# Kernel tuning notes

Measured on AMD Instinct MI355X. Metric: run time of the kernel, lower is better.

## Reference

```python
import jax, jax.numpy as jnp
import numpy as np

N = 262144      # total line-graph nodes (16 graphs x 16384)
E = 2097152     # total line-graph edges (avg degree 8)
F_IN = 8        # edge_attr feature dim
FEATURES_DIM = 64


def gcn_conv(x, src, dst, W, b, n):
    """PyG GCNConv: x' = D^{-1/2} (A+I) D^{-1/2} (x W) + b, deg from in-edges incl. self-loops."""
    x = x @ W
    loop = jnp.arange(n, dtype=src.dtype)
    si = jnp.concatenate([src, loop])
    di = jnp.concatenate([dst, loop])
    deg = jax.ops.segment_sum(jnp.ones(si.shape[0], dtype=x.dtype), di, num_segments=n)
    dinv = jnp.where(deg > 0, deg ** -0.5, 0.0)
    norm = dinv[si] * dinv[di]                      # [E+N]
    msg = x[si] * norm[:, None]                     # gather + scale
    return jax.ops.segment_sum(msg, di, num_segments=n) + b


def setup_inputs() -> dict:
    key = jax.random.key(0)
    ks = jax.random.split(key, 10)

    def lin(k, fan_in, fan_out):
        return jax.random.normal(k, (fan_in, fan_out), jnp.float32) * (1.0 / np.sqrt(fan_in))

    return {
        "x": jax.random.normal(ks[0], (N, F_IN), jnp.float32),
        "W1": lin(ks[1], F_IN, 16), "b1": jnp.zeros((16,), jnp.float32),
        "W2": lin(ks[2], 16, 32),   "b2": jnp.zeros((32,), jnp.float32),
        "W3": lin(ks[3], 32, 64),   "b3": jnp.zeros((64,), jnp.float32),
        "Wfc": lin(ks[4], 64, FEATURES_DIM), "bfc": jnp.zeros((FEATURES_DIM,), jnp.float32),
        "edge_index": jax.random.randint(ks[5], (2, E), 0, N, dtype=jnp.int32),
        "batch_size": 16,
    }


def reference(x, W1, b1, W2, b2, W3, b3, Wfc, bfc, edge_index, batch_size):
    src, dst = edge_index[0], edge_index[1]
    n = x.shape[0]
    h = jax.nn.relu(gcn_conv(x, src, dst, W1, b1, n))
    h = jax.nn.relu(gcn_conv(h, src, dst, W2, b2, n))
    h = jax.nn.relu(gcn_conv(h, src, dst, W3, b3, n))
    out = h @ Wfc + bfc
    return out.reshape(batch_size, -1, FEATURES_DIM)
```

## Files before the change

### kernel.cpp

```cpp
#include <hip/hip_runtime.h>
#include <hip/hip_bf16.h>


#define NB   256
#define NPB  1024
#define TILE 4096
#define SRCMASK 0x3FFFFu

typedef _Float16 half8 __attribute__((ext_vector_type(8)));
typedef float float4v __attribute__((ext_vector_type(4)));
typedef unsigned int u32x4 __attribute__((ext_vector_type(4)));

__device__ __forceinline__ unsigned pkh(float a, float b) {
    unsigned short ua = __builtin_bit_cast(unsigned short, (_Float16)a);
    unsigned short ub = __builtin_bit_cast(unsigned short, (_Float16)b);
    return (unsigned)ua | ((unsigned)ub << 16);
}
__device__ __forceinline__ float h_lo(unsigned u) {
    return (float)__builtin_bit_cast(_Float16, (unsigned short)(u & 0xFFFFu));
}
__device__ __forceinline__ float h_hi(unsigned u) {
    return (float)__builtin_bit_cast(_Float16, (unsigned short)(u >> 16));
}
__device__ __forceinline__ int ld_nt(const int* p) { return __builtin_nontemporal_load(p); }

#define UNPK8_ADD(A, u) \
    A##0 += h_lo(u.x); A##1 += h_hi(u.x); A##2 += h_lo(u.y); A##3 += h_hi(u.y); \
    A##4 += h_lo(u.z); A##5 += h_hi(u.z); A##6 += h_lo(u.w); A##7 += h_hi(u.w);

__global__ void hist_kernel(const int* __restrict__ dst, int* __restrict__ ghist,
                            int E, int shift) {
    __shared__ int h[NB];
    int tid = threadIdx.x;
    h[tid] = 0;
    __syncthreads();
    int base = blockIdx.x * TILE;
    int cnt = min(TILE, E - base);
    for (int i = tid; i < cnt; i += 256)
        atomicAdd(&h[dst[base + i] >> shift], 1);
    __syncthreads();
    int v = h[tid];
    if (v) atomicAdd(&ghist[tid], v);
}

__global__ void bscan_kernel(const int* __restrict__ ghist, int* __restrict__ bbase,
                             int* __restrict__ gcursor,
                             const float* __restrict__ W3, const float* __restrict__ Wf,
                             _Float16* __restrict__ w3f, _Float16* __restrict__ wff) {
    __shared__ int sh[NB];
    int tid = threadIdx.x;
    int v = ghist[tid];
    sh[tid] = v;
    __syncthreads();
    for (int o = 1; o < NB; o <<= 1) {
        int t = (tid >= o) ? sh[tid - o] : 0;
        __syncthreads();
        sh[tid] += t;
        __syncthreads();
    }
    int incl = sh[tid];
    bbase[tid] = incl - v;
    gcursor[tid] = incl - v;
    if (tid == NB - 1) bbase[NB] = incl;
    for (int i = tid; i < 32 * 64; i += NB) {
        int k = i >> 6, j = i & 63;
        w3f[(j >> 4) * 512 + (j & 15) * 32 + (k >> 3) * 8 + (k & 7)] = (_Float16)W3[i];
    }
    for (int i = tid; i < 64 * 64; i += NB) {
        int k = i >> 6, j = i & 63;
        wff[((k >> 5) * 4 + (j >> 4)) * 512 + (j & 15) * 32 + ((k >> 3) & 3) * 8 + (k & 7)]
            = (_Float16)Wf[i];
    }
}

__global__ void __launch_bounds__(256)
partition_kernel(const int* __restrict__ src, const int* __restrict__ dst,
                 int* __restrict__ gcursor, unsigned int* __restrict__ bedge,
                 int E, int shift, int mask) {
    __shared__ int h[NB], st[NB], gp[NB];
    __shared__ unsigned short rk[TILE];
    __shared__ int sd[TILE];
    __shared__ int ss[TILE];
    int tid = threadIdx.x;
    h[tid] = 0;
    __syncthreads();
    int base = blockIdx.x * TILE;
    int cnt = min(TILE, E - base);
    for (int i = tid; i < cnt; i += 256)
        rk[i] = (unsigned short)atomicAdd(&h[dst[base + i] >> shift], 1);
    __syncthreads();
    int hv = h[tid];
    st[tid] = hv;
    __syncthreads();
    for (int o = 1; o < NB; o <<= 1) {
        int t = (tid >= o) ? st[tid - o] : 0;
        __syncthreads();
        st[tid] += t;
        __syncthreads();
    }
    st[tid] -= hv;
    gp[tid] = hv ? atomicAdd(&gcursor[tid], hv) : 0;
    __syncthreads();
    for (int i = tid; i < cnt; i += 256) {
        int d = dst[base + i];
        int b = d >> shift;
        int pos = st[b] + rk[i];
        sd[pos] = d;
        ss[pos] = src[base + i];
    }
    __syncthreads();
    for (int i = tid; i < cnt; i += 256) {
        int d = sd[i];
        int b = d >> shift;
        int g = gp[b] + (i - st[b]);
        bedge[g] = (unsigned int)ss[i] | ((unsigned int)(d & mask) << 18);
    }
}

__global__ void __launch_bounds__(256)
build_kernel(const int* __restrict__ bbase, const unsigned int* __restrict__ bedge,
             const float* __restrict__ x,
             int* __restrict__ off, float* __restrict__ dinv, int* __restrict__ adj,
             _Float16* __restrict__ y0h) {
    __shared__ int deg1[NPB];
    __shared__ int cur[NPB];
    __shared__ int bs[256];
    int tid = threadIdx.x;
    int b = blockIdx.x;
    int s = bbase[b], e = bbase[b + 1];
    int base = tid * 4;
#pragma unroll
    for (int i = 0; i < 4; i++) deg1[base + i] = 0;
    __syncthreads();
    for (int i = s + tid; i < e; i += 256)
        atomicAdd(&deg1[bedge[i] >> 18], 1);
    __syncthreads();
    int d0 = deg1[base], d1 = deg1[base + 1], d2 = deg1[base + 2], d3 = deg1[base + 3];
    int th = d0 + d1 + d2 + d3;
    bs[tid] = th;
    __syncthreads();
    for (int o = 1; o < 256; o <<= 1) {
        int t = (tid >= o) ? bs[tid - o] : 0;
        __syncthreads();
        bs[tid] += t;
        __syncthreads();
    }
    int run = s + bs[tid] - th;
    int vb = b * NPB + base;
    off[vb]     = run; cur[base]     = run; dinv[vb]     = rsqrtf((float)(d0 + 1)); run += d0;
    off[vb + 1] = run; cur[base + 1] = run; dinv[vb + 1] = rsqrtf((float)(d1 + 1)); run += d1;
    off[vb + 2] = run; cur[base + 2] = run; dinv[vb + 2] = rsqrtf((float)(d2 + 1)); run += d2;
    off[vb + 3] = run; cur[base + 3] = run; dinv[vb + 3] = rsqrtf((float)(d3 + 1)); run += d3;
    if (b == NB - 1 && tid == 255) off[NB * NPB] = e;
    __syncthreads();
    for (int i = s + tid; i < e; i += 256) {
        unsigned int pk = bedge[i];
        int p = atomicAdd(&cur[pk >> 18], 1);
        adj[p] = (int)(pk & SRCMASK);
    }
    for (int i = tid; i < NPB; i += 256) {
        float dv = rsqrtf((float)(deg1[i] + 1));
        const float4* xr = (const float4*)x + (size_t)(b * NPB + i) * 2;
        float4 t0 = xr[0], t1 = xr[1];
        uint4 pk;
        pk.x = pkh(t0.x * dv, t0.y * dv); pk.y = pkh(t0.z * dv, t0.w * dv);
        pk.z = pkh(t1.x * dv, t1.y * dv); pk.w = pkh(t1.z * dv, t1.w * dv);
        ((uint4*)y0h)[(size_t)b * NPB + i] = pk;
    }
}

__global__ void __launch_bounds__(256)
aggt1_kernel(const _Float16* __restrict__ y0h, const int* __restrict__ off,
             const int* __restrict__ adj, const float* __restrict__ dinv,
             const float* __restrict__ W1, const float* __restrict__ b1,
             _Float16* __restrict__ y1h) {
    __shared__ float Ws[8 * 16];
    __shared__ float bsh[16];
    const int tid = threadIdx.x;
    if (tid < 128) Ws[tid] = W1[tid];
    if (tid < 16) bsh[tid] = b1[tid];
    const int vg = blockIdx.x * 256 + tid;
    const u32x4* y4 = (const u32x4*)y0h;
    int beg = off[vg], end = off[vg + 1];
    u32x4 us = y4[vg];
    float a0 = h_lo(us.x), a1 = h_hi(us.x), a2 = h_lo(us.y), a3 = h_hi(us.y),
          a4 = h_lo(us.z), a5 = h_hi(us.z), a6 = h_lo(us.w), a7 = h_hi(us.w);
    float c0 = 0, c1 = 0, c2 = 0, c3 = 0, c4 = 0, c5 = 0, c6 = 0, c7 = 0;
    u32x4 zz; zz.x = 0; zz.y = 0; zz.z = 0; zz.w = 0;
    for (int eb = beg; eb < end; eb += 8) {
        int i0 = ld_nt(adj + eb);
        int i1 = ld_nt(adj + min(eb + 1, end - 1));
        int i2 = ld_nt(adj + min(eb + 2, end - 1));
        int i3 = ld_nt(adj + min(eb + 3, end - 1));
        int i4 = ld_nt(adj + min(eb + 4, end - 1));
        int i5 = ld_nt(adj + min(eb + 5, end - 1));
        int i6 = ld_nt(adj + min(eb + 6, end - 1));
        int i7 = ld_nt(adj + min(eb + 7, end - 1));
        u32x4 u0 = y4[i0], u1 = y4[i1], u2 = y4[i2], u3 = y4[i3];
        u32x4 u4 = y4[i4], u5 = y4[i5], u6 = y4[i6], u7 = y4[i7];
        u1 = (eb + 1 < end) ? u1 : zz;
        u2 = (eb + 2 < end) ? u2 : zz;
        u3 = (eb + 3 < end) ? u3 : zz;
        u4 = (eb + 4 < end) ? u4 : zz;
        u5 = (eb + 5 < end) ? u5 : zz;
        u6 = (eb + 6 < end) ? u6 : zz;
        u7 = (eb + 7 < end) ? u7 : zz;
        UNPK8_ADD(a, u0) UNPK8_ADD(c, u1) UNPK8_ADD(a, u2) UNPK8_ADD(c, u3)
        UNPK8_ADD(a, u4) UNPK8_ADD(c, u5) UNPK8_ADD(a, u6) UNPK8_ADD(c, u7)
    }
    float dv = dinv[vg];
    float in[8];
    in[0] = (a0 + c0) * dv; in[1] = (a1 + c1) * dv;
    in[2] = (a2 + c2) * dv; in[3] = (a3 + c3) * dv;
    in[4] = (a4 + c4) * dv; in[5] = (a5 + c5) * dv;
    in[6] = (a6 + c6) * dv; in[7] = (a7 + c7) * dv;
    __syncthreads();
    const float4* W4 = (const float4*)Ws;
    float o[16];
    {
        float4 b0 = ((const float4*)bsh)[0], b1v = ((const float4*)bsh)[1];
        float4 b2v = ((const float4*)bsh)[2], b3v = ((const float4*)bsh)[3];
        o[0] = b0.x; o[1] = b0.y; o[2] = b0.z; o[3] = b0.w;
        o[4] = b1v.x; o[5] = b1v.y; o[6] = b1v.z; o[7] = b1v.w;
        o[8] = b2v.x; o[9] = b2v.y; o[10] = b2v.z; o[11] = b2v.w;
        o[12] = b3v.x; o[13] = b3v.y; o[14] = b3v.z; o[15] = b3v.w;
    }
#pragma unroll
    for (int k = 0; k < 8; k++) {
        float xk = in[k];
        float4 w0 = W4[k * 4 + 0], w1 = W4[k * 4 + 1];
        float4 w2 = W4[k * 4 + 2], w3 = W4[k * 4 + 3];
        o[0] = fmaf(xk, w0.x, o[0]);  o[1] = fmaf(xk, w0.y, o[1]);
        o[2] = fmaf(xk, w0.z, o[2]);  o[3] = fmaf(xk, w0.w, o[3]);
        o[4] = fmaf(xk, w1.x, o[4]);  o[5] = fmaf(xk, w1.y, o[5]);
        o[6] = fmaf(xk, w1.z, o[6]);  o[7] = fmaf(xk, w1.w, o[7]);
        o[8] = fmaf(xk, w2.x, o[8]);  o[9] = fmaf(xk, w2.y, o[9]);
        o[10] = fmaf(xk, w2.z, o[10]); o[11] = fmaf(xk, w2.w, o[11]);
        o[12] = fmaf(xk, w3.x, o[12]); o[13] = fmaf(xk, w3.y, o[13]);
        o[14] = fmaf(xk, w3.z, o[14]); o[15] = fmaf(xk, w3.w, o[15]);
    }
    uint4 p0, p1;
    p0.x = pkh(dv * fmaxf(o[0], 0.f),  dv * fmaxf(o[1], 0.f));
    p0.y = pkh(dv * fmaxf(o[2], 0.f),  dv * fmaxf(o[3], 0.f));
    p0.z = pkh(dv * fmaxf(o[4], 0.f),  dv * fmaxf(o[5], 0.f));
    p0.w = pkh(dv * fmaxf(o[6], 0.f),  dv * fmaxf(o[7], 0.f));
    p1.x = pkh(dv * fmaxf(o[8], 0.f),  dv * fmaxf(o[9], 0.f));
    p1.y = pkh(dv * fmaxf(o[10], 0.f), dv * fmaxf(o[11], 0.f));
    p1.z = pkh(dv * fmaxf(o[12], 0.f), dv * fmaxf(o[13], 0.f));
    p1.w = pkh(dv * fmaxf(o[14], 0.f), dv * fmaxf(o[15], 0.f));
    uint4* out4 = (uint4*)y1h;
    out4[(size_t)vg * 2]     = p0;
    out4[(size_t)vg * 2 + 1] = p1;
}

__global__ void __launch_bounds__(256)
aggt2_kernel(const _Float16* __restrict__ y1h, const int* __restrict__ off,
             const int* __restrict__ adj, const float* __restrict__ dinv,
             const float* __restrict__ W2, const float* __restrict__ b2,
             unsigned int* __restrict__ y2b) {
    __shared__ float Ws[16 * 32];
    __shared__ float bsh[32];
    const int tid = threadIdx.x;
    for (int i = tid; i < 16 * 32; i += 256) Ws[i] = W2[i];
    if (tid < 32) bsh[tid] = b2[tid];
    const int vbase = blockIdx.x * 128;
    const int vl = tid >> 1, c = tid & 1;
    const int vg = vbase + vl;
    const u32x4* y4 = (const u32x4*)y1h;
    int beg = off[vg], end = off[vg + 1];
    u32x4 us = y4[(size_t)vg * 2 + c];
    float a0 = h_lo(us.x), a1 = h_hi(us.x), a2 = h_lo(us.y), a3 = h_hi(us.y),
          a4 = h_lo(us.z), a5 = h_hi(us.z), a6 = h_lo(us.w), a7 = h_hi(us.w);
    float c0 = 0, c1 = 0, c2 = 0, c3 = 0, c4 = 0, c5 = 0, c6 = 0, c7 = 0;
    u32x4 zz; zz.x = 0; zz.y = 0; zz.z = 0; zz.w = 0;
    for (int eb = beg; eb < end; eb += 8) {
        int i0 = ld_nt(adj + eb);
        int i1 = ld_nt(adj + min(eb + 1, end - 1));
        int i2 = ld_nt(adj + min(eb + 2, end - 1));
        int i3 = ld_nt(adj + min(eb + 3, end - 1));
        int i4 = ld_nt(adj + min(eb + 4, end - 1));
        int i5 = ld_nt(adj + min(eb + 5, end - 1));
        int i6 = ld_nt(adj + min(eb + 6, end - 1));
        int i7 = ld_nt(adj + min(eb + 7, end - 1));
        u32x4 u0 = y4[(size_t)i0 * 2 + c], u1 = y4[(size_t)i1 * 2 + c];
        u32x4 u2 = y4[(size_t)i2 * 2 + c], u3 = y4[(size_t)i3 * 2 + c];
        u32x4 u4 = y4[(size_t)i4 * 2 + c], u5 = y4[(size_t)i5 * 2 + c];
        u32x4 u6 = y4[(size_t)i6 * 2 + c], u7 = y4[(size_t)i7 * 2 + c];
        u1 = (eb + 1 < end) ? u1 : zz;
        u2 = (eb + 2 < end) ? u2 : zz;
        u3 = (eb + 3 < end) ? u3 : zz;
        u4 = (eb + 4 < end) ? u4 : zz;
        u5 = (eb + 5 < end) ? u5 : zz;
        u6 = (eb + 6 < end) ? u6 : zz;
        u7 = (eb + 7 < end) ? u7 : zz;
        UNPK8_ADD(a, u0) UNPK8_ADD(c, u1) UNPK8_ADD(a, u2) UNPK8_ADD(c, u3)
        UNPK8_ADD(a, u4) UNPK8_ADD(c, u5) UNPK8_ADD(a, u6) UNPK8_ADD(c, u7)
    }
    float dv = dinv[vg];
    float own[8];
    own[0] = (a0 + c0) * dv; own[1] = (a1 + c1) * dv;
    own[2] = (a2 + c2) * dv; own[3] = (a3 + c3) * dv;
    own[4] = (a4 + c4) * dv; own[5] = (a5 + c5) * dv;
    own[6] = (a6 + c6) * dv; own[7] = (a7 + c7) * dv;
    float oth[8];
#pragma unroll
    for (int k = 0; k < 8; k++) oth[k] = __shfl_xor(own[k], 1);
    float in[16];
#pragma unroll
    for (int k = 0; k < 8; k++) {
        in[c * 8 + k] = own[k];
        in[(1 - c) * 8 + k] = oth[k];
    }
    __syncthreads();
    const int j0 = c * 16;
    const float4* W4 = (const float4*)Ws;
    float o[16];
#pragma unroll
    for (int jj = 0; jj < 16; jj += 4) {
        float4 bv = *(const float4*)&bsh[j0 + jj];
        o[jj] = bv.x; o[jj + 1] = bv.y; o[jj + 2] = bv.z; o[jj + 3] = bv.w;
    }
#pragma unroll
    for (int k = 0; k < 16; k++) {
        float xk = in[k];
        float4 w0 = W4[k * 8 + c * 4 + 0], w1 = W4[k * 8 + c * 4 + 1];
        float4 w2 = W4[k * 8 + c * 4 + 2], w3 = W4[k * 8 + c * 4 + 3];
        o[0] = fmaf(xk, w0.x, o[0]);  o[1] = fmaf(xk, w0.y, o[1]);
        o[2] = fmaf(xk, w0.z, o[2]);  o[3] = fmaf(xk, w0.w, o[3]);
        o[4] = fmaf(xk, w1.x, o[4]);  o[5] = fmaf(xk, w1.y, o[5]);
        o[6] = fmaf(xk, w1.z, o[6]);  o[7] = fmaf(xk, w1.w, o[7]);
        o[8] = fmaf(xk, w2.x, o[8]);  o[9] = fmaf(xk, w2.y, o[9]);
        o[10] = fmaf(xk, w2.z, o[10]); o[11] = fmaf(xk, w2.w, o[11]);
        o[12] = fmaf(xk, w3.x, o[12]); o[13] = fmaf(xk, w3.y, o[13]);
        o[14] = fmaf(xk, w3.z, o[14]); o[15] = fmaf(xk, w3.w, o[15]);
    }
    uint4 p0, p1;
    p0.x = pkh(dv * fmaxf(o[0], 0.f),  dv * fmaxf(o[1], 0.f));
    p0.y = pkh(dv * fmaxf(o[2], 0.f),  dv * fmaxf(o[3], 0.f));
    p0.z = pkh(dv * fmaxf(o[4], 0.f),  dv * fmaxf(o[5], 0.f));
    p0.w = pkh(dv * fmaxf(o[6], 0.f),  dv * fmaxf(o[7], 0.f));
    p1.x = pkh(dv * fmaxf(o[8], 0.f),  dv * fmaxf(o[9], 0.f));
    p1.y = pkh(dv * fmaxf(o[10], 0.f), dv * fmaxf(o[11], 0.f));
    p1.z = pkh(dv * fmaxf(o[12], 0.f), dv * fmaxf(o[13], 0.f));
    p1.w = pkh(dv * fmaxf(o[14], 0.f), dv * fmaxf(o[15], 0.f));
    uint4* out4 = (uint4*)y2b;
    out4[(size_t)vg * 4 + c * 2]     = p0;
    out4[(size_t)vg * 4 + c * 2 + 1] = p1;
}

__global__ void __launch_bounds__(256)
agg3_kernel(const unsigned int* __restrict__ y2b, const int* __restrict__ off,
            const int* __restrict__ adj, const float* __restrict__ dinv,
            _Float16* __restrict__ a3out, int n) {
    int t = blockIdx.x * 256 + threadIdx.x;
    int v = t >> 2, c = t & 3;
    if (v >= n) return;
    const u32x4* yb = (const u32x4*)y2b;
    u32x4 us = yb[(size_t)v * 4 + c];
    float a0 = h_lo(us.x), a1 = h_hi(us.x), a2 = h_lo(us.y), a3 = h_hi(us.y),
          a4 = h_lo(us.z), a5 = h_hi(us.z), a6 = h_lo(us.w), a7 = h_hi(us.w);
    float c0 = 0, c1 = 0, c2 = 0, c3 = 0, c4 = 0, c5 = 0, c6 = 0, c7 = 0;
    int beg = off[v], end = off[v + 1];
    u32x4 zz; zz.x = 0; zz.y = 0; zz.z = 0; zz.w = 0;
    for (int eb = beg; eb < end; eb += 8) {
        int i0 = ld_nt(adj + eb);
        int i1 = ld_nt(adj + min(eb + 1, end - 1));
        int i2 = ld_nt(adj + min(eb + 2, end - 1));
        int i3 = ld_nt(adj + min(eb + 3, end - 1));
        int i4 = ld_nt(adj + min(eb + 4, end - 1));
        int i5 = ld_nt(adj + min(eb + 5, end - 1));
        int i6 = ld_nt(adj + min(eb + 6, end - 1));
        int i7 = ld_nt(adj + min(eb + 7, end - 1));
        u32x4 u0 = yb[(size_t)i0 * 4 + c], u1 = yb[(size_t)i1 * 4 + c];
        u32x4 u2 = yb[(size_t)i2 * 4 + c], u3 = yb[(size_t)i3 * 4 + c];
        u32x4 u4 = yb[(size_t)i4 * 4 + c], u5 = yb[(size_t)i5 * 4 + c];
        u32x4 u6 = yb[(size_t)i6 * 4 + c], u7 = yb[(size_t)i7 * 4 + c];
        u1 = (eb + 1 < end) ? u1 : zz;
        u2 = (eb + 2 < end) ? u2 : zz;
        u3 = (eb + 3 < end) ? u3 : zz;
        u4 = (eb + 4 < end) ? u4 : zz;
        u5 = (eb + 5 < end) ? u5 : zz;
        u6 = (eb + 6 < end) ? u6 : zz;
        u7 = (eb + 7 < end) ? u7 : zz;
        UNPK8_ADD(a, u0) UNPK8_ADD(c, u1) UNPK8_ADD(a, u2) UNPK8_ADD(c, u3)
        UNPK8_ADD(a, u4) UNPK8_ADD(c, u5) UNPK8_ADD(a, u6) UNPK8_ADD(c, u7)
    }
    float dv = dinv[v];
    u32x4 st;
    st.x = pkh((a0 + c0) * dv, (a1 + c1) * dv);
    st.y = pkh((a2 + c2) * dv, (a3 + c3) * dv);
    st.z = pkh((a4 + c4) * dv, (a5 + c5) * dv);
    st.w = pkh((a6 + c6) * dv, (a7 + c7) * dv);
    ((u32x4*)a3out)[(size_t)v * 4 + c] = st;
}

__global__ void __launch_bounds__(256)
t3fc_kernel(const _Float16* __restrict__ a3h,
            const _Float16* __restrict__ w3f, const float* __restrict__ b3,
            const _Float16* __restrict__ wff, const float* __restrict__ bf,
            float* __restrict__ out) {
    __shared__ __align__(16) _Float16 tA[4][1024];
    const int tid = threadIdx.x;
    const int w = tid >> 6, l = tid & 63;
    const int lr = l & 15, lh = l >> 4;
    const int vbase = blockIdx.x * 64 + w * 16;
    const int fragoff = lr * 32 + lh * 8;

    half8 A1 = *(const half8*)(a3h + (size_t)(vbase + lr) * 32 + lh * 8);

    float4v c1[4];
#pragma unroll
    for (int nt = 0; nt < 4; nt++) {
        float bv = b3[nt * 16 + lr];
        float4v ci = {bv, bv, bv, bv};
        half8 B = *(const half8*)(w3f + nt * 512 + fragoff);
        c1[nt] = __builtin_amdgcn_mfma_f32_16x16x32_f16(A1, B, ci, 0, 0, 0);
    }

    _Float16* tw = tA[w];
#pragma unroll
    for (int nt = 0; nt < 4; nt++) {
        int k2 = nt * 16 + lr;
        int base = (k2 >> 5) * 512 + ((k2 >> 3) & 3) * 8 + (k2 & 7);
#pragma unroll
        for (int r = 0; r < 4; r++)
            tw[base + (lh * 4 + r) * 32] = (_Float16)fmaxf(c1[nt][r], 0.f);
    }

    float4v c2[4];
#pragma unroll
    for (int nt = 0; nt < 4; nt++) {
        float bv = bf[nt * 16 + lr];
        c2[nt] = (float4v){bv, bv, bv, bv};
    }
#pragma unroll
    for (int ks = 0; ks < 2; ks++) {
        half8 A2 = *(const half8*)(tw + ks * 512 + fragoff);
#pragma unroll
        for (int nt = 0; nt < 4; nt++) {
            half8 B = *(const half8*)(wff + (ks * 4 + nt) * 512 + fragoff);
            c2[nt] = __builtin_amdgcn_mfma_f32_16x16x32_f16(A2, B, c2[nt], 0, 0, 0);
        }
    }

#pragma unroll
    for (int nt = 0; nt < 4; nt++) {
#pragma unroll
        for (int r = 0; r < 4; r++)
            out[(size_t)(vbase + lh * 4 + r) * 64 + nt * 16 + lr] = c2[nt][r];
    }
}

extern "C" void kernel_launch(void* const* d_in, const int* in_sizes, int n_in,
                              void* d_out, int out_size, void* d_ws, size_t ws_size,
                              hipStream_t stream) {
    const float* x  = (const float*)d_in[0];
    const float* W1 = (const float*)d_in[1];
    const float* b1 = (const float*)d_in[2];
    const float* W2 = (const float*)d_in[3];
    const float* b2 = (const float*)d_in[4];
    const float* W3 = (const float*)d_in[5];
    const float* b3 = (const float*)d_in[6];
    const float* Wf = (const float*)d_in[7];
    const float* bf = (const float*)d_in[8];
    const int*   ei = (const int*)d_in[9];

    const int N = in_sizes[0] / 8;
    const int E = in_sizes[9] / 2;
    const int* srcv = ei;
    const int* dstv = ei + E;
    const int shift = 10;

    char* p = (char*)d_ws;
    auto take = [&p](size_t bytes) { char* q = p; p += (bytes + 63) & ~size_t(63); return q; };
    int*   off   = (int*)take((size_t)(N + 16) * 4);
    float* dinv  = (float*)take((size_t)N * 4);
    int*   adj   = (int*)take((size_t)E * 4);
    int*   ghist = (int*)take(NB * 4);
    int*   bbase = (int*)take((NB + 1) * 4);
    int*   gcur  = (int*)take(NB * 4);
    _Float16* w3f = (_Float16*)take(32 * 64 * 2);
    _Float16* wff = (_Float16*)take(64 * 64 * 2);
    char*  bufA  = take((size_t)N * 32 * 4);
    char*  bufB  = take((size_t)N * 16 * 4);
    char*  regX  = take((size_t)N * 32 * 2);
    unsigned int* bedge = (unsigned int*)regX;
    unsigned int* y2b   = (unsigned int*)regX;
    _Float16* y0h = (_Float16*)bufA;
    _Float16* a3h = (_Float16*)bufA;
    _Float16* y1h = (_Float16*)bufB;

    hipMemsetAsync(ghist, 0, NB * 4, stream);

    int nt = (E + TILE - 1) / TILE;
    hist_kernel<<<nt, 256, 0, stream>>>(dstv, ghist, E, shift);
    bscan_kernel<<<1, NB, 0, stream>>>(ghist, bbase, gcur, W3, Wf, w3f, wff);
    partition_kernel<<<nt, 256, 0, stream>>>(srcv, dstv, gcur, bedge, E, shift, NPB - 1);
    build_kernel<<<NB, 256, 0, stream>>>(bbase, bedge, x, off, dinv, adj, y0h);

    aggt1_kernel<<<N / 256, 256, 0, stream>>>(y0h, off, adj, dinv, W1, b1, y1h);
    aggt2_kernel<<<N / 128, 256, 0, stream>>>(y1h, off, adj, dinv, W2, b2, y2b);
    agg3_kernel<<<(N * 4) / 256, 256, 0, stream>>>(y2b, off, adj, dinv, a3h, N);
    t3fc_kernel<<<N / 64, 256, 0, stream>>>(a3h, w3f, b3, wff, bf, (float*)d_out);
}
```

Measured before the change: 285.9 us.

## Fuse layer-3 aggregation into MFMA transform kernel; one node per thread in layer 2

The layer-3 neighbour aggregation now writes its normalized fp16 result straight into shared memory, where the MFMA layer-3 and FC transform reads it. This removes a separate kernel launch and an N x 32 fp16 round trip through global memory. Layer-2 aggregation changes from two threads per node, which split the 16 features and exchanged them with shuffles, to one thread per node that gathers all 16 features and computes all 32 outputs. That removes the shuffles and the duplicated index loads but raises register pressure and halves the thread count.

```diff
diff --git a/kernel.cpp b/kernel.cpp
--- a/kernel.cpp
+++ b/kernel.cpp
@@ -27,6 +27,12 @@
 #define UNPK8_ADD(A, u) \
     A##0 += h_lo(u.x); A##1 += h_hi(u.x); A##2 += h_lo(u.y); A##3 += h_hi(u.y); \
     A##4 += h_lo(u.z); A##5 += h_hi(u.z); A##6 += h_lo(u.w); A##7 += h_hi(u.w);
+
+#define UNPK16_ARR(A, ul, uh) \
+    A[0] += h_lo(ul.x); A[1] += h_hi(ul.x); A[2] += h_lo(ul.y); A[3] += h_hi(ul.y); \
+    A[4] += h_lo(ul.z); A[5] += h_hi(ul.z); A[6] += h_lo(ul.w); A[7] += h_hi(ul.w); \
+    A[8] += h_lo(uh.x); A[9] += h_hi(uh.x); A[10] += h_lo(uh.y); A[11] += h_hi(uh.y); \
+    A[12] += h_lo(uh.z); A[13] += h_hi(uh.z); A[14] += h_lo(uh.w); A[15] += h_hi(uh.w);
 
 __global__ void hist_kernel(const int* __restrict__ dst, int* __restrict__ ghist,
                             int E, int shift) {
@@ -263,150 +269,127 @@
     const int tid = threadIdx.x;
     for (int i = tid; i < 16 * 32; i += 256) Ws[i] = W2[i];
     if (tid < 32) bsh[tid] = b2[tid];
-    const int vbase = blockIdx.x * 128;
-    const int vl = tid >> 1, c = tid & 1;
-    const int vg = vbase + vl;
+    const int vg = blockIdx.x * 256 + tid;
     const u32x4* y4 = (const u32x4*)y1h;
     int beg = off[vg], end = off[vg + 1];
-    u32x4 us = y4[(size_t)vg * 2 + c];
-    float a0 = h_lo(us.x), a1 = h_hi(us.x), a2 = h_lo(us.y), a3 = h_hi(us.y),
-          a4 = h_lo(us.z), a5 = h_hi(us.z), a6 = h_lo(us.w), a7 = h_hi(us.w);
-    float c0 = 0, c1 = 0, c2 = 0, c3 = 0, c4 = 0, c5 = 0, c6 = 0, c7 = 0;
+    float A[16], C[16];
+#pragma unroll
+    for (int k = 0; k < 16; k++) { A[k] = 0.f; C[k] = 0.f; }
+    {
+        u32x4 usl = y4[(size_t)vg * 2], ush = y4[(size_t)vg * 2 + 1];
+        UNPK16_ARR(A, usl, ush)
+    }
     u32x4 zz; zz.x = 0; zz.y = 0; zz.z = 0; zz.w = 0;
-    for (int eb = beg; eb < end; eb += 8) {
+    for (int eb = beg; eb < end; eb += 4) {
         int i0 = ld_nt(adj + eb);
         int i1 = ld_nt(adj + min(eb + 1, end - 1));
         int i2 = ld_nt(adj + min(eb + 2, end - 1));
         int i3 = ld_nt(adj + min(eb + 3, end - 1));
-        int i4 = ld_nt(adj + min(eb + 4, end - 1));
-        int i5 = ld_nt(adj + min(eb + 5, end - 1));
-        int i6 = ld_nt(adj + min(eb + 6, end - 1));
-        int i7 = ld_nt(adj + min(eb + 7, end - 1));
-        u32x4 u0 = y4[(size_t)i0 * 2 + c], u1 = y4[(size_t)i1 * 2 + c];
-        u32x4 u2 = y4[(size_t)i2 * 2 + c], u3 = y4[(size_t)i3 * 2 + c];
-        u32x4 u4 = y4[(size_t)i4 * 2 + c], u5 = y4[(size_t)i5 * 2 + c];
-        u32x4 u6 = y4[(size_t)i6 * 2 + c], u7 = y4[(size_t)i7 * 2 + c];
-        u1 = (eb + 1 < end) ? u1 : zz;
-        u2 = (eb + 2 < end) ? u2 : zz;
-        u3 = (eb + 3 < end) ? u3 : zz;
-        u4 = (eb + 4 < end) ? u4 : zz;
-        u5 = (eb + 5 < end) ? u5 : zz;
-        u6 = (eb + 6 < end) ? u6 : zz;
-        u7 = (eb + 7 < end) ? u7 : zz;
-        UNPK8_ADD(a, u0) UNPK8_ADD(c, u1) UNPK8_ADD(a, u2) UNPK8_ADD(c, u3)
-        UNPK8_ADD(a, u4) UNPK8_ADD(c, u5) UNPK8_ADD(a, u6) UNPK8_ADD(c, u7)
+        u32x4 u0l = y4[(size_t)i0 * 2], u0h = y4[(size_t)i0 * 2 + 1];
+        u32x4 u1l = y4[(size_t)i1 * 2], u1h = y4[(size_t)i1 * 2 + 1];
+        u32x4 u2l = y4[(size_t)i2 * 2], u2h = y4[(size_t)i2 * 2 + 1];
+        u32x4 u3l = y4[(size_t)i3 * 2], u3h = y4[(size_t)i3 * 2 + 1];
+        bool m1 = eb + 1 < end, m2 = eb + 2 < end, m3 = eb + 3 < end;
+        u1l = m1 ? u1l : zz; u1h = m1 ? u1h : zz;
+        u2l = m2 ? u2l : zz; u2h = m2 ? u2h : zz;
+        u3l = m3 ? u3l : zz; u3h = m3 ? u3h : zz;
+        UNPK16_ARR(A, u0l, u0h) UNPK16_ARR(C, u1l, u1h)
+        UNPK16_ARR(A, u2l, u2h) UNPK16_ARR(C, u3l, u3h)
     }
     float dv = dinv[vg];
-    float own[8];
-    own[0] = (a0 + c0) * dv; own[1] = (a1 + c1) * dv;
-    own[2] = (a2 + c2) * dv; own[3] = (a3 + c3) * dv;
-    own[4] = (a4 + c4) * dv; own[5] = (a5 + c5) * dv;
-    own[6] = (a6 + c6) * dv; own[7] = (a7 + c7) * dv;
-    float oth[8];
-#pragma unroll
-    for (int k = 0; k < 8; k++) oth[k] = __shfl_xor(own[k], 1);
     float in[16];
 #pragma unroll
-    for (int k = 0; k < 8; k++) {
-        in[c * 8 + k] = own[k];
-        in[(1 - c) * 8 + k] = oth[k];
-    }
-    __syncthreads();
-    const int j0 = c * 16;
+    for (int k = 0; k < 16; k++) in[k] = (A[k] + C[k]) * dv;
+    __syncthreads();
     const float4* W4 = (const float4*)Ws;
-    float o[16];
-#pragma unroll
-    for (int jj = 0; jj < 16; jj += 4) {
-        float4 bv = *(const float4*)&bsh[j0 + jj];
+    float o[32];
+#pragma unroll
+    for (int jj = 0; jj < 32; jj += 4) {
+        float4 bv = *(const float4*)&bsh[jj];
         o[jj] = bv.x; o[jj + 1] = bv.y; o[jj + 2] = bv.z; o[jj + 3] = bv.w;
     }
 #pragma unroll
     for (int k = 0; k < 16; k++) {
         float xk = in[k];
-        float4 w0 = W4[k * 8 + c * 4 + 0], w1 = W4[k * 8 + c * 4 + 1];
-        float4 w2 = W4[k * 8 + c * 4 + 2], w3 = W4[k * 8 + c * 4 + 3];
-        o[0] = fmaf(xk, w0.x, o[0]);  o[1] = fmaf(xk, w0.y, o[1]);
-        o[2] = fmaf(xk, w0.z, o[2]);  o[3] = fmaf(xk, w0.w, o[3]);
-        o[4] = fmaf(xk, w1.x, o[4]);  o[5] = fmaf(xk, w1.y, o[5]);
-        o[6] = fmaf(xk, w1.z, o[6]);  o[7] = fmaf(xk, w1.w, o[7]);
-        o[8] = fmaf(xk, w2.x, o[8]);  o[9] = fmaf(xk, w2.y, o[9]);
-        o[10] = fmaf(xk, w2.z, o[10]); o[11] = fmaf(xk, w2.w, o[11]);
-        o[12] = fmaf(xk, w3.x, o[12]); o[13] = fmaf(xk, w3.y, o[13]);
-        o[14] = fmaf(xk, w3.z, o[14]); o[15] = fmaf(xk, w3.w, o[15]);
-    }
-    uint4 p0, p1;
-    p0.x = pkh(dv * fmaxf(o[0], 0.f),  dv * fmaxf(o[1], 0.f));
-    p0.y = pkh(dv * fmaxf(o[2], 0.f),  dv * fmaxf(o[3], 0.f));
-    p0.z = pkh(dv * fmaxf(o[4], 0.f),  dv * fmaxf(o[5], 0.f));
-    p0.w = pkh(dv * fmaxf(o[6], 0.f),  dv * fmaxf(o[7], 0.f));
-    p1.x = pkh(dv * fmaxf(o[8], 0.f),  dv * fmaxf(o[9], 0.f));
-    p1.y = pkh(dv * fmaxf(o[10], 0.f), dv * fmaxf(o[11], 0.f));
-    p1.z = pkh(dv * fmaxf(o[12], 0.f), dv * fmaxf(o[13], 0.f));
-    p1.w = pkh(dv * fmaxf(o[14], 0.f), dv * fmaxf(o[15], 0.f));
-    uint4* out4 = (uint4*)y2b;
-    out4[(size_t)vg * 4 + c * 2]     = p0;
-    out4[(size_t)vg * 4 + c * 2 + 1] = p1;
-}
-
+#pragma unroll
+        for (int q = 0; q < 8; q++) {
+            float4 w = W4[k * 8 + q];
+            o[q * 4 + 0] = fmaf(xk, w.x, o[q * 4 + 0]);
+            o[q * 4 + 1] = fmaf(xk, w.y, o[q * 4 + 1]);
+            o[q * 4 + 2] = fmaf(xk, w.z, o[q * 4 + 2]);
+            o[q * 4 + 3] = fmaf(xk, w.w, o[q * 4 + 3]);
+        }
+    }
+    u32x4* out4 = (u32x4*)y2b + (size_t)vg * 4;
+#pragma unroll
+    for (int q = 0; q < 4; q++) {
+        u32x4 pk;
+        pk.x = pkh(dv * fmaxf(o[q * 8 + 0], 0.f), dv * fmaxf(o[q * 8 + 1], 0.f));
+        pk.y = pkh(dv * fmaxf(o[q * 8 + 2], 0.f), dv * fmaxf(o[q * 8 + 3], 0.f));
+        pk.z = pkh(dv * fmaxf(o[q * 8 + 4], 0.f), dv * fmaxf(o[q * 8 + 5], 0.f));
+        pk.w = pkh(dv * fmaxf(o[q * 8 + 6], 0.f), dv * fmaxf(o[q * 8 + 7], 0.f));
+        out4[q] = pk;
+    }
+}
+
+#define TIN_P 40
 __global__ void __launch_bounds__(256)
-agg3_kernel(const unsigned int* __restrict__ y2b, const int* __restrict__ off,
-            const int* __restrict__ adj, const float* __restrict__ dinv,
-            _Float16* __restrict__ a3out, int n) {
-    int t = blockIdx.x * 256 + threadIdx.x;
-    int v = t >> 2, c = t & 3;
-    if (v >= n) return;
-    const u32x4* yb = (const u32x4*)y2b;
-    u32x4 us = yb[(size_t)v * 4 + c];
-    float a0 = h_lo(us.x), a1 = h_hi(us.x), a2 = h_lo(us.y), a3 = h_hi(us.y),
-          a4 = h_lo(us.z), a5 = h_hi(us.z), a6 = h_lo(us.w), a7 = h_hi(us.w);
-    float c0 = 0, c1 = 0, c2 = 0, c3 = 0, c4 = 0, c5 = 0, c6 = 0, c7 = 0;
-    int beg = off[v], end = off[v + 1];
-    u32x4 zz; zz.x = 0; zz.y = 0; zz.z = 0; zz.w = 0;
-    for (int eb = beg; eb < end; eb += 8) {
-        int i0 = ld_nt(adj + eb);
-        int i1 = ld_nt(adj + min(eb + 1, end - 1));
-        int i2 = ld_nt(adj + min(eb + 2, end - 1));
-        int i3 = ld_nt(adj + min(eb + 3, end - 1));
-        int i4 = ld_nt(adj + min(eb + 4, end - 1));
-        int i5 = ld_nt(adj + min(eb + 5, end - 1));
-        int i6 = ld_nt(adj + min(eb + 6, end - 1));
-        int i7 = ld_nt(adj + min(eb + 7, end - 1));
-        u32x4 u0 = yb[(size_t)i0 * 4 + c], u1 = yb[(size_t)i1 * 4 + c];
-        u32x4 u2 = yb[(size_t)i2 * 4 + c], u3 = yb[(size_t)i3 * 4 + c];
-        u32x4 u4 = yb[(size_t)i4 * 4 + c], u5 = yb[(size_t)i5 * 4 + c];
-        u32x4 u6 = yb[(size_t)i6 * 4 + c], u7 = yb[(size_t)i7 * 4 + c];
-        u1 = (eb + 1 < end) ? u1 : zz;
-        u2 = (eb + 2 < end) ? u2 : zz;
-        u3 = (eb + 3 < end) ? u3 : zz;
-        u4 = (eb + 4 < end) ? u4 : zz;
-        u5 = (eb + 5 < end) ? u5 : zz;
-        u6 = (eb + 6 < end) ? u6 : zz;
-        u7 = (eb + 7 < end) ? u7 : zz;
-        UNPK8_ADD(a, u0) UNPK8_ADD(c, u1) UNPK8_ADD(a, u2) UNPK8_ADD(c, u3)
-        UNPK8_ADD(a, u4) UNPK8_ADD(c, u5) UNPK8_ADD(a, u6) UNPK8_ADD(c, u7)
-    }
-    float dv = dinv[v];
-    u32x4 st;
-    st.x = pkh((a0 + c0) * dv, (a1 + c1) * dv);
-    st.y = pkh((a2 + c2) * dv, (a3 + c3) * dv);
-    st.z = pkh((a4 + c4) * dv, (a5 + c5) * dv);
-    st.w = pkh((a6 + c6) * dv, (a7 + c7) * dv);
-    ((u32x4*)a3out)[(size_t)v * 4 + c] = st;
-}
-
-__global__ void __launch_bounds__(256)
-t3fc_kernel(const _Float16* __restrict__ a3h,
-            const _Float16* __restrict__ w3f, const float* __restrict__ b3,
-            const _Float16* __restrict__ wff, const float* __restrict__ bf,
-            float* __restrict__ out) {
+agg3t3fc_kernel(const unsigned int* __restrict__ y2b, const int* __restrict__ off,
+                const int* __restrict__ adj, const float* __restrict__ dinv,
+                const _Float16* __restrict__ w3f, const float* __restrict__ b3,
+                const _Float16* __restrict__ wff, const float* __restrict__ bf,
+                float* __restrict__ out) {
+    __shared__ __align__(16) _Float16 tin[4][16 * TIN_P];
     __shared__ __align__(16) _Float16 tA[4][1024];
     const int tid = threadIdx.x;
     const int w = tid >> 6, l = tid & 63;
+    const int vbase = blockIdx.x * 64 + w * 16;
+
+    {
+        const int nl = l >> 2, c = l & 3;
+        const int v = vbase + nl;
+        const u32x4* yb = (const u32x4*)y2b;
+        u32x4 us = yb[(size_t)v * 4 + c];
+        float a0 = h_lo(us.x), a1 = h_hi(us.x), a2 = h_lo(us.y), a3 = h_hi(us.y),
+              a4 = h_lo(us.z), a5 = h_hi(us.z), a6 = h_lo(us.w), a7 = h_hi(us.w);
+        float c0 = 0, c1 = 0, c2 = 0, c3 = 0, c4 = 0, c5 = 0, c6 = 0, c7 = 0;
+        int beg = off[v], end = off[v + 1];
+        u32x4 zz; zz.x = 0; zz.y = 0; zz.z = 0; zz.w = 0;
+        for (int eb = beg; eb < end; eb += 8) {
+            int i0 = ld_nt(adj + eb);
+            int i1 = ld_nt(adj + min(eb + 1, end - 1));
+            int i2 = ld_nt(adj + min(eb + 2, end - 1));
+            int i3 = ld_nt(adj + min(eb + 3, end - 1));
+            int i4 = ld_nt(adj + min(eb + 4, end - 1));
+            int i5 = ld_nt(adj + min(eb + 5, end - 1));
+            int i6 = ld_nt(adj + min(eb + 6, end - 1));
+            int i7 = ld_nt(adj + min(eb + 7, end - 1));
+            u32x4 u0 = yb[(size_t)i0 * 4 + c], u1 = yb[(size_t)i1 * 4 + c];
+            u32x4 u2 = yb[(size_t)i2 * 4 + c], u3 = yb[(size_t)i3 * 4 + c];
+            u32x4 u4 = yb[(size_t)i4 * 4 + c], u5 = yb[(size_t)i5 * 4 + c];
+            u32x4 u6 = yb[(size_t)i6 * 4 + c], u7 = yb[(size_t)i7 * 4 + c];
+            u1 = (eb + 1 < end) ? u1 : zz;
+            u2 = (eb + 2 < end) ? u2 : zz;
+            u3 = (eb + 3 < end) ? u3 : zz;
+            u4 = (eb + 4 < end) ? u4 : zz;
+            u5 = (eb + 5 < end) ? u5 : zz;
+            u6 = (eb + 6 < end) ? u6 : zz;
+            u7 = (eb + 7 < end) ? u7 : zz;
+            UNPK8_ADD(a, u0) UNPK8_ADD(c, u1) UNPK8_ADD(a, u2) UNPK8_ADD(c, u3)
+            UNPK8_ADD(a, u4) UNPK8_ADD(c, u5) UNPK8_ADD(a, u6) UNPK8_ADD(c, u7)
+        }
+        float dv = dinv[v];
+        u32x4 pk;
+        pk.x = pkh((a0 + c0) * dv, (a1 + c1) * dv);
+        pk.y = pkh((a2 + c2) * dv, (a3 + c3) * dv);
+        pk.z = pkh((a4 + c4) * dv, (a5 + c5) * dv);
+        pk.w = pkh((a6 + c6) * dv, (a7 + c7) * dv);
+        *(u32x4*)(tin[w] + nl * TIN_P + c * 8) = pk;
+    }
+
     const int lr = l & 15, lh = l >> 4;
-    const int vbase = blockIdx.x * 64 + w * 16;
     const int fragoff = lr * 32 + lh * 8;
-
-    half8 A1 = *(const half8*)(a3h + (size_t)(vbase + lr) * 32 + lh * 8);
+    half8 A1 = *(const half8*)(tin[w] + lr * TIN_P + lh * 8);
 
     float4v c1[4];
 #pragma unroll
@@ -487,7 +470,6 @@
     unsigned int* bedge = (unsigned int*)regX;
     unsigned int* y2b   = (unsigned int*)regX;
     _Float16* y0h = (_Float16*)bufA;
-    _Float16* a3h = (_Float16*)bufA;
     _Float16* y1h = (_Float16*)bufB;
 
     hipMemsetAsync(ghist, 0, NB * 4, stream);
@@ -499,7 +481,7 @@
     build_kernel<<<NB, 256, 0, stream>>>(bbase, bedge, x, off, dinv, adj, y0h);
 
     aggt1_kernel<<<N / 256, 256, 0, stream>>>(y0h, off, adj, dinv, W1, b1, y1h);
-    aggt2_kernel<<<N / 128, 256, 0, stream>>>(y1h, off, adj, dinv, W2, b2, y2b);
-    agg3_kernel<<<(N * 4) / 256, 256, 0, stream>>>(y2b, off, adj, dinv, a3h, N);
-    t3fc_kernel<<<N / 64, 256, 0, stream>>>(a3h, w3f, b3, wff, bf, (float*)d_out);
-}
+    aggt2_kernel<<<N / 256, 256, 0, stream>>>(y1h, off, adj, dinv, W2, b2, y2b);
+    agg3t3fc_kernel<<<N / 64, 256, 0, stream>>>(y2b, off, adj, dinv, w3f, b3, wff, bf,
+                                                (float*)d_out);
+}
```

New measurement: 280.9 us. No clear change (-1.7%).
